# Performance work log

Measured on AMD Instinct MI355X. Metric: run time of the kernel, lower is better.

Reference implementation:

```python
import jax, jax.numpy as jnp
import numpy as np

B, T, I, H, O = 8192, 1024, 2, 10, 2


def _gru_scan(gates_x, W_hh, b_hh, collect):
    """gates_x: [B,T,3H] precomputed input-side gates. Returns outputs [B,T,H] if collect else final h [B,H]."""
    def step(h, gx):
        gh = h @ W_hh.T + b_hh                      # [B,3H]
        xr, xz, xn = jnp.split(gx, 3, axis=-1)
        hr, hz, hn = jnp.split(gh, 3, axis=-1)
        r = jax.nn.sigmoid(xr + hr)
        z = jax.nn.sigmoid(xz + hz)
        n = jnp.tanh(xn + r * hn)
        h_new = (1.0 - z) * n + z * h
        return h_new, (h_new if collect else None)
    h0 = jnp.zeros((gates_x.shape[0], W_hh.shape[1]), gates_x.dtype)
    hT, ys = jax.lax.scan(step, h0, jnp.swapaxes(gates_x, 0, 1))  # scan over time
    return jnp.swapaxes(ys, 0, 1) if collect else hT


def setup_inputs() -> dict:
    key = jax.random.key(0)
    ks = jax.random.split(key, 12)
    s = 1.0 / np.sqrt(H)  # PyTorch GRU/Linear init scale
    u = lambda k, shp: jax.random.uniform(k, shp, jnp.float32, -s, s)
    return {
        "batchX": jax.random.normal(ks[0], (B, T, I), jnp.float32),
        "W_ih0": u(ks[1], (3 * H, I)),  "W_hh0": u(ks[2], (3 * H, H)),
        "b_ih0": u(ks[3], (3 * H,)),    "b_hh0": u(ks[4], (3 * H,)),
        "W_ih1": u(ks[5], (3 * H, H)),  "W_hh1": u(ks[6], (3 * H, H)),
        "b_ih1": u(ks[7], (3 * H,)),    "b_hh1": u(ks[8], (3 * H,)),
        "W_fc": u(ks[9], (O, H)),       "b_fc": u(ks[10], (O,)),
    }


def reference(batchX, W_ih0, W_hh0, b_ih0, b_hh0, W_ih1, W_hh1, b_ih1, b_hh1, W_fc, b_fc):
    # Layer 0: need full sequence of hidden states (feeds layer 1)
    gx0 = batchX @ W_ih0.T + b_ih0                  # [B,T,3H] one big GEMM
    h1 = _gru_scan(gx0, W_hh0, b_hh0, collect=True)  # [B,T,H]
    # Layer 1: only final hidden state is used by the head
    gx1 = h1 @ W_ih1.T + b_ih1                      # [B,T,3H]
    hT = _gru_scan(gx1, W_hh1, b_hh1, collect=False)  # [B,H]
    return hT @ W_fc.T + b_fc                       # [B,O]
```

## Files before the change

kernel.cpp:

```cpp
#include <hip/hip_runtime.h>

#define NB 8192
#define NT 1024
#define NH 10
#define ROWS_PER_WAVE 4
#define ROWS_PER_BLOCK 16

typedef float v2f __attribute__((ext_vector_type(2)));
typedef float v4f __attribute__((ext_vector_type(4)));

#define LOG2E 1.44269504088896340736f

__device__ __forceinline__ float rcpf(float x) { return __builtin_amdgcn_rcpf(x); }
__device__ __forceinline__ float exp2i(float x) {
    float r;
    asm("v_exp_f32 %0, %1" : "=v"(r) : "v"(x));
    return r;
}
__device__ __forceinline__ float tanh2u(float u) { return fmaf(-2.0f, rcpf(exp2i(u) + 1.0f), 1.0f); }
__device__ __forceinline__ void sigm2q2(float qa, float qb, float& sa, float& sb) {
    const float da = 1.0f + exp2i(qa);
    const float db = 1.0f + exp2i(qb);
    const float R = rcpf(da * db);
    sa = db * R;
    sb = da * R;
}

__device__ __forceinline__ v2f lo2(v4f a) { return __builtin_shufflevector(a, a, 0, 1); }
__device__ __forceinline__ v2f hi2(v4f a) { return __builtin_shufflevector(a, a, 2, 3); }
__device__ __forceinline__ v2f pkfma(v2f a, v2f b, v2f c) {
    return __builtin_elementwise_fma(a, b, c);
}

struct W5 { v2f p[5]; };
__device__ __forceinline__ W5 loadrow_scaled(const float* __restrict__ q, float s) {
    W5 w;
#pragma unroll
    for (int k = 0; k < 5; ++k) w.p[k] = (v2f){q[2 * k] * s, q[2 * k + 1] * s};
    return w;
}
__device__ __forceinline__ v2f dotWacc(const W5& w, v4f ha, v4f hb, v2f hc, v2f acc) {
    acc = pkfma(w.p[0], lo2(ha), acc);
    acc = pkfma(w.p[1], hi2(ha), acc);
    acc = pkfma(w.p[2], lo2(hb), acc);
    acc = pkfma(w.p[3], hi2(hb), acc);
    acc = pkfma(w.p[4], hc, acc);
    return acc;
}
__device__ __forceinline__ float hsum(v2f a) { return a.x + a.y; }

__global__ __launch_bounds__(256) void gru_fused(
    const float* __restrict__ X,
    const float* __restrict__ Wih0, const float* __restrict__ Whh0,
    const float* __restrict__ bih0, const float* __restrict__ bhh0,
    const float* __restrict__ Wih1, const float* __restrict__ Whh1,
    const float* __restrict__ bih1, const float* __restrict__ bhh1,
    const float* __restrict__ Wfc,  const float* __restrict__ bfc,
    float* __restrict__ out)
{
    __shared__ __align__(16) float hls[4][2][5][12];

    const int tid  = threadIdx.x;
    const int lane = tid & 63;
    const int wave = tid >> 6;
    const int g    = lane / 10;
    const int j    = lane - g * 10;
    const int gg   = (g < 4) ? g : 4;

    const bool active = (g < ROWS_PER_WAVE);
    int b = blockIdx.x * ROWS_PER_BLOCK + wave * ROWS_PER_WAVE + (active ? g : 0);
    const bool store_ok = active && (b < NB);
    if (b >= NB) b = NB - 1;

    const int r0 = j, r1 = j + 10, r2 = j + 20;
    const float Sz = -LOG2E;
    const float Sn = 2.0f * LOG2E;

    const v2f wxr = (v2f){Wih0[r0 * 2] * Sz, Wih0[r0 * 2 + 1] * Sz};
    const v2f wxz = (v2f){Wih0[r1 * 2] * Sz, Wih0[r1 * 2 + 1] * Sz};
    const v2f wxn = (v2f){Wih0[r2 * 2] * Sn, Wih0[r2 * 2 + 1] * Sn};

    const W5 whr0 = loadrow_scaled(Whh0 + r0 * NH, Sz);
    const W5 whz0 = loadrow_scaled(Whh0 + r1 * NH, Sz);
    const W5 whn0 = loadrow_scaled(Whh0 + r2 * NH, Sn);
    const W5 wir1 = loadrow_scaled(Wih1 + r0 * NH, Sz);
    const W5 wiz1 = loadrow_scaled(Wih1 + r1 * NH, Sz);
    const W5 win1 = loadrow_scaled(Wih1 + r2 * NH, Sn);
    const W5 whr1 = loadrow_scaled(Whh1 + r0 * NH, Sz);
    const W5 whz1 = loadrow_scaled(Whh1 + r1 * NH, Sz);
    const W5 whn1 = loadrow_scaled(Whh1 + r2 * NH, Sn);

    const float br0  = (bih0[r0] + bhh0[r0]) * Sz;
    const float bz0  = (bih0[r1] + bhh0[r1]) * Sz;
    const float bxn0 = bih0[r2] * Sn;
    const float bhn0 = bhh0[r2] * Sn;
    const float br1  = (bih1[r0] + bhh1[r0]) * Sz;
    const float bz1  = (bih1[r1] + bhh1[r1]) * Sz;
    const float bxn1 = bih1[r2] * Sn;
    const float bhn1 = bhh1[r2] * Sn;

    float* const L0 = &hls[wave][0][gg][0];
    float* const L1 = &hls[wave][1][gg][0];

    v4f h0a = (v4f){0,0,0,0}, h0b = (v4f){0,0,0,0}; v2f h0c = (v2f){0,0};
    v4f h1a = (v4f){0,0,0,0}, h1b = (v4f){0,0,0,0}; v2f h1c = (v2f){0,0};
    float my0 = 0.0f, my1 = 0.0f;

    const float2* xp = reinterpret_cast<const float2*>(X) + (size_t)b * NT;
    float2 xc = xp[0];
    float2 xn2;

#define STEP(DO_PREFETCH, T)                                                    \
    do {                                                                        \
        if (DO_PREFETCH) xn2 = xp[(T) + 1];                                     \
        const v2f xv = (v2f){xc.x, xc.y};                                       \
                                             \
        v2f accr = pkfma(wxr, xv, (v2f){br0, 0.0f});                            \
        v2f accz = pkfma(wxz, xv, (v2f){bz0, 0.0f});                            \
        v2f accx = pkfma(wxn, xv, (v2f){bxn0, 0.0f});                           \
        accr = dotWacc(whr0, h0a, h0b, h0c, accr);                              \
        accz = dotWacc(whz0, h0a, h0b, h0c, accz);                              \
        const v2f acch = dotWacc(whn0, h0a, h0b, h0c, (v2f){bhn0, 0.0f});       \
        float r, z;                                                             \
        sigm2q2(hsum(accr), hsum(accz), r, z);                                  \
        const float n = tanh2u(fmaf(r, hsum(acch), hsum(accx)));                \
        my0 = fmaf(z, my0 - n, n);                                              \
           \
           \
        L0[j] = my0;                                                            \
        const v4f nh0a = *reinterpret_cast<const v4f*>(L0);                     \
        const v4f nh0b = *reinterpret_cast<const v4f*>(L0 + 4);                 \
        const v2f nh0c = *reinterpret_cast<const v2f*>(L0 + 8);                 \
                    \
        v2f aqr = dotWacc(whr1, h1a, h1b, h1c, (v2f){br1, 0.0f});               \
        v2f aqz = dotWacc(whz1, h1a, h1b, h1c, (v2f){bz1, 0.0f});               \
        const v2f aqh = dotWacc(whn1, h1a, h1b, h1c, (v2f){bhn1, 0.0f});        \
           \
        h0a = nh0a; h0b = nh0b; h0c = nh0c;                                     \
        aqr = dotWacc(wir1, h0a, h0b, h0c, aqr);                                \
        aqz = dotWacc(wiz1, h0a, h0b, h0c, aqz);                                \
        const v2f aqx = dotWacc(win1, h0a, h0b, h0c, (v2f){bxn1, 0.0f});        \
        float r1v, z1v;                                                         \
        sigm2q2(hsum(aqr), hsum(aqz), r1v, z1v);                                \
        const float n1v = tanh2u(fmaf(r1v, hsum(aqh), hsum(aqx)));              \
        my1 = fmaf(z1v, my1 - n1v, n1v);                                        \
        L1[j] = my1;                                                            \
        h1a = *reinterpret_cast<const v4f*>(L1);                                \
        h1b = *reinterpret_cast<const v4f*>(L1 + 4);                            \
        h1c = *reinterpret_cast<const v2f*>(L1 + 8);                            \
        if (DO_PREFETCH) xc = xn2;                                              \
    } while (0)

    for (int t = 0; t < NT - 1; ++t) {
        STEP(true, t);
    }
    STEP(false, NT - 1);
#undef STEP

    if (store_ok && j < 2) {
        const W5 wf = loadrow_scaled(Wfc + j * NH, 1.0f);
        out[(size_t)b * 2 + j] = hsum(dotWacc(wf, h1a, h1b, h1c, (v2f){bfc[j], 0.0f}));
    }
}

extern "C" void kernel_launch(void* const* d_in, const int* in_sizes, int n_in,
                              void* d_out, int out_size, void* d_ws, size_t ws_size,
                              hipStream_t stream) {
    const float* X    = (const float*)d_in[0];
    const float* Wih0 = (const float*)d_in[1];
    const float* Whh0 = (const float*)d_in[2];
    const float* bih0 = (const float*)d_in[3];
    const float* bhh0 = (const float*)d_in[4];
    const float* Wih1 = (const float*)d_in[5];
    const float* Whh1 = (const float*)d_in[6];
    const float* bih1 = (const float*)d_in[7];
    const float* bhh1 = (const float*)d_in[8];
    const float* Wfc  = (const float*)d_in[9];
    const float* bfc  = (const float*)d_in[10];
    float* out = (float*)d_out;

    const int grid = NB / ROWS_PER_BLOCK;
    gru_fused<<<grid, 256, 0, stream>>>(X, Wih0, Whh0, bih0, bhh0,
                                        Wih1, Whh1, bih1, bhh1, Wfc, bfc, out);
}
```

Before: 427.1 us.

## Software-pipeline layer-1 GRU step one timestep behind layer-0

Restructures the time loop so that layer 0 at step t runs in the same iteration as layer 1 at step t-1, with a prologue and epilogue. The two layers' independent math can then interleave and hide the LDS round-trip latency of each layer's hidden-state exchange. It also swaps the inline-asm v_exp for the compiler builtin so the scheduler can reorder it, and turns the biases into vector constants. The cost is higher register pressure and a loop that is harder to follow.

```diff
diff --git a/kernel.cpp b/kernel.cpp
--- a/kernel.cpp
+++ b/kernel.cpp
@@ -13,9 +13,13 @@
 
 __device__ __forceinline__ float rcpf(float x) { return __builtin_amdgcn_rcpf(x); }
 __device__ __forceinline__ float exp2i(float x) {
+#if __has_builtin(__builtin_amdgcn_exp2f)
+    return __builtin_amdgcn_exp2f(x);
+#else
     float r;
     asm("v_exp_f32 %0, %1" : "=v"(r) : "v"(x));
     return r;
+#endif
 }
 __device__ __forceinline__ float tanh2u(float u) { return fmaf(-2.0f, rcpf(exp2i(u) + 1.0f), 1.0f); }
 __device__ __forceinline__ void sigm2q2(float qa, float qb, float& sa, float& sb) {
@@ -90,72 +94,88 @@
     const W5 whz1 = loadrow_scaled(Whh1 + r1 * NH, Sz);
     const W5 whn1 = loadrow_scaled(Whh1 + r2 * NH, Sn);
 
-    const float br0  = (bih0[r0] + bhh0[r0]) * Sz;
-    const float bz0  = (bih0[r1] + bhh0[r1]) * Sz;
-    const float bxn0 = bih0[r2] * Sn;
-    const float bhn0 = bhh0[r2] * Sn;
-    const float br1  = (bih1[r0] + bhh1[r0]) * Sz;
-    const float bz1  = (bih1[r1] + bhh1[r1]) * Sz;
-    const float bxn1 = bih1[r2] * Sn;
-    const float bhn1 = bhh1[r2] * Sn;
+    const v2f sr0 = (v2f){(bih0[r0] + bhh0[r0]) * Sz, 0.0f};
+    const v2f sz0 = (v2f){(bih0[r1] + bhh0[r1]) * Sz, 0.0f};
+    const v2f sx0 = (v2f){bih0[r2] * Sn, 0.0f};
+    const v2f sh0 = (v2f){bhh0[r2] * Sn, 0.0f};
+    const v2f sr1 = (v2f){(bih1[r0] + bhh1[r0]) * Sz, 0.0f};
+    const v2f sz1 = (v2f){(bih1[r1] + bhh1[r1]) * Sz, 0.0f};
+    const v2f sx1 = (v2f){bih1[r2] * Sn, 0.0f};
+    const v2f sh1 = (v2f){bhh1[r2] * Sn, 0.0f};
 
     float* const L0 = &hls[wave][0][gg][0];
     float* const L1 = &hls[wave][1][gg][0];
 
     v4f h0a = (v4f){0,0,0,0}, h0b = (v4f){0,0,0,0}; v2f h0c = (v2f){0,0};
-    v4f h1a = (v4f){0,0,0,0}, h1b = (v4f){0,0,0,0}; v2f h1c = (v2f){0,0};
+    v4f h1a, h1b; v2f h1c;
+    v4f nh1a = (v4f){0,0,0,0}, nh1b = (v4f){0,0,0,0}; v2f nh1c = (v2f){0,0};
     float my0 = 0.0f, my1 = 0.0f;
 
     const float2* xp = reinterpret_cast<const float2*>(X) + (size_t)b * NT;
     float2 xc = xp[0];
     float2 xn2;
 
-#define STEP(DO_PREFETCH, T)                                                    \
-    do {                                                                        \
-        if (DO_PREFETCH) xn2 = xp[(T) + 1];                                     \
-        const v2f xv = (v2f){xc.x, xc.y};                                       \
-                                             \
-        v2f accr = pkfma(wxr, xv, (v2f){br0, 0.0f});                            \
-        v2f accz = pkfma(wxz, xv, (v2f){bz0, 0.0f});                            \
-        v2f accx = pkfma(wxn, xv, (v2f){bxn0, 0.0f});                           \
-        accr = dotWacc(whr0, h0a, h0b, h0c, accr);                              \
-        accz = dotWacc(whz0, h0a, h0b, h0c, accz);                              \
-        const v2f acch = dotWacc(whn0, h0a, h0b, h0c, (v2f){bhn0, 0.0f});       \
-        float r, z;                                                             \
-        sigm2q2(hsum(accr), hsum(accz), r, z);                                  \
-        const float n = tanh2u(fmaf(r, hsum(acch), hsum(accx)));                \
-        my0 = fmaf(z, my0 - n, n);                                              \
-           \
-           \
-        L0[j] = my0;                                                            \
-        const v4f nh0a = *reinterpret_cast<const v4f*>(L0);                     \
-        const v4f nh0b = *reinterpret_cast<const v4f*>(L0 + 4);                 \
-        const v2f nh0c = *reinterpret_cast<const v2f*>(L0 + 8);                 \
-                    \
-        v2f aqr = dotWacc(whr1, h1a, h1b, h1c, (v2f){br1, 0.0f});               \
-        v2f aqz = dotWacc(whz1, h1a, h1b, h1c, (v2f){bz1, 0.0f});               \
-        const v2f aqh = dotWacc(whn1, h1a, h1b, h1c, (v2f){bhn1, 0.0f});        \
-           \
-        h0a = nh0a; h0b = nh0b; h0c = nh0c;                                     \
-        aqr = dotWacc(wir1, h0a, h0b, h0c, aqr);                                \
-        aqz = dotWacc(wiz1, h0a, h0b, h0c, aqz);                                \
-        const v2f aqx = dotWacc(win1, h0a, h0b, h0c, (v2f){bxn1, 0.0f});        \
-        float r1v, z1v;                                                         \
-        sigm2q2(hsum(aqr), hsum(aqz), r1v, z1v);                                \
-        const float n1v = tanh2u(fmaf(r1v, hsum(aqh), hsum(aqx)));              \
-        my1 = fmaf(z1v, my1 - n1v, n1v);                                        \
-        L1[j] = my1;                                                            \
-        h1a = *reinterpret_cast<const v4f*>(L1);                                \
-        h1b = *reinterpret_cast<const v4f*>(L1 + 4);                            \
-        h1c = *reinterpret_cast<const v2f*>(L1 + 8);                            \
-        if (DO_PREFETCH) xc = xn2;                                              \
-    } while (0)
-
-    for (int t = 0; t < NT - 1; ++t) {
-        STEP(true, t);
-    }
-    STEP(false, NT - 1);
-#undef STEP
+    v2f accr, accz, accx, acch, aqr, aqz, aqx, aqh;
+    v4f nh0a, nh0b; v2f nh0c;
+    float r0v, z0v, n0v, r1v, z1v, n1v;
+
+#define L0_GATES(xv)                                                            \
+    accr = pkfma(wxr, xv, sr0);                                                 \
+    accz = pkfma(wxz, xv, sz0);                                                 \
+    accx = pkfma(wxn, xv, sx0);                                                 \
+    accr = dotWacc(whr0, h0a, h0b, h0c, accr);                                  \
+    accz = dotWacc(whz0, h0a, h0b, h0c, accz);                                  \
+    acch = dotWacc(whn0, h0a, h0b, h0c, sh0);                                   \
+    sigm2q2(hsum(accr), hsum(accz), r0v, z0v);                                  \
+    n0v = tanh2u(fmaf(r0v, hsum(acch), hsum(accx)));                            \
+    my0 = fmaf(z0v, my0 - n0v, n0v);                                            \
+    L0[j] = my0;                                                                \
+    nh0a = *reinterpret_cast<const v4f*>(L0);                                   \
+    nh0b = *reinterpret_cast<const v4f*>(L0 + 4);                               \
+    nh0c = *reinterpret_cast<const v2f*>(L0 + 8)
+
+#define L1_GATES()                                                              \
+    aqr = dotWacc(whr1, h1a, h1b, h1c, sr1);                                    \
+    aqz = dotWacc(whz1, h1a, h1b, h1c, sz1);                                    \
+    aqh = dotWacc(whn1, h1a, h1b, h1c, sh1);                                    \
+    aqr = dotWacc(wir1, h0a, h0b, h0c, aqr);                                    \
+    aqz = dotWacc(wiz1, h0a, h0b, h0c, aqz);                                    \
+    aqx = dotWacc(win1, h0a, h0b, h0c, sx1);                                    \
+    sigm2q2(hsum(aqr), hsum(aqz), r1v, z1v);                                    \
+    n1v = tanh2u(fmaf(r1v, hsum(aqh), hsum(aqx)));                              \
+    my1 = fmaf(z1v, my1 - n1v, n1v)
+
+    {
+        const v2f xv = (v2f){xc.x, xc.y};
+        L0_GATES(xv);
+        h0a = nh0a; h0b = nh0b; h0c = nh0c;
+        xc = xp[1];
+    }
+
+    for (int t = 1; t < NT; ++t) {
+        xn2 = xp[(t + 1 < NT) ? (t + 1) : (NT - 1)];
+        const v2f xv = (v2f){xc.x, xc.y};
+        L0_GATES(xv);
+        h1a = nh1a; h1b = nh1b; h1c = nh1c;
+        L1_GATES();
+        h0a = nh0a; h0b = nh0b; h0c = nh0c;
+        L1[j] = my1;
+        nh1a = *reinterpret_cast<const v4f*>(L1);
+        nh1b = *reinterpret_cast<const v4f*>(L1 + 4);
+        nh1c = *reinterpret_cast<const v2f*>(L1 + 8);
+        xc = xn2;
+    }
+
+    {
+        h1a = nh1a; h1b = nh1b; h1c = nh1c;
+        L1_GATES();
+        L1[j] = my1;
+        h1a = *reinterpret_cast<const v4f*>(L1);
+        h1b = *reinterpret_cast<const v4f*>(L1 + 4);
+        h1c = *reinterpret_cast<const v2f*>(L1 + 8);
+    }
+#undef L0_GATES
+#undef L1_GATES
 
     if (store_ok && j < 2) {
         const W5 wf = loadrow_scaled(Wfc + j * NH, 1.0f);
```

Result: faster. 414.3 us (-3.0%).
